# Kernel optimization log

Measured on AMD Instinct MI355X. Metric: run time of the kernel, lower is better.

Reference implementation:

```python
import jax, jax.numpy as jnp
import numpy as np

DEPTH, HEADS, DIM, MLP = 4, 8, 256, 1024
EPS = 1e-5


def setup_inputs() -> dict:
    key = jax.random.key(0)
    ks = jax.random.split(key, 12)
    s = 0.02
    return {
        "x": jax.random.normal(ks[0], (4, 2048, DIM), dtype=jnp.float32),
        "ln1_g": jnp.ones((DEPTH, DIM), jnp.float32),
        "ln1_b": jnp.zeros((DEPTH, DIM), jnp.float32),
        "w_qkv": jax.random.normal(ks[1], (DEPTH, DIM, 3 * DIM), jnp.float32) * s,
        "w_out": jax.random.normal(ks[2], (DEPTH, DIM, DIM), jnp.float32) * s,
        "b_out": jnp.zeros((DEPTH, DIM), jnp.float32),
        "ln2_g": jnp.ones((DEPTH, DIM), jnp.float32),
        "ln2_b": jnp.zeros((DEPTH, DIM), jnp.float32),
        "w1": jax.random.normal(ks[3], (DEPTH, DIM, MLP), jnp.float32) * s,
        "b1": jnp.zeros((DEPTH, MLP), jnp.float32),
        "w2": jax.random.normal(ks[4], (DEPTH, MLP, DIM), jnp.float32) * s,
        "b2": jnp.zeros((DEPTH, DIM), jnp.float32),
    }


def _layernorm(x, g, b):
    m = jnp.mean(x, axis=-1, keepdims=True)
    v = jnp.mean(jnp.square(x - m), axis=-1, keepdims=True)
    return (x - m) * jax.lax.rsqrt(v + EPS) * g + b


def _attention(x, w_qkv, w_out, b_out):
    b, n, d = x.shape
    h = HEADS
    scale = d ** (-0.5)  # NOTE: module scales by dim**-0.5, not head_dim**-0.5
    qkv = x @ w_qkv  # [b, n, 3*d]
    qkv = qkv.reshape(b, n, 3, h, d // h)
    q, k, v = jnp.moveaxis(qkv, 2, 0)  # each [b, n, h, hd]
    q = jnp.swapaxes(q, 1, 2)  # [b, h, n, hd]
    k = jnp.swapaxes(k, 1, 2)
    v = jnp.swapaxes(v, 1, 2)
    dots = jnp.einsum('bhid,bhjd->bhij', q, k) * scale
    attn = jax.nn.softmax(dots, axis=-1)
    out = jnp.einsum('bhij,bhjd->bhid', attn, v)
    out = jnp.swapaxes(out, 1, 2).reshape(b, n, d)
    return out @ w_out + b_out


def _ffn(x, w1, b1, w2, b2):
    return jax.nn.gelu(x @ w1 + b1, approximate=False) @ w2 + b2


def reference(x, ln1_g, ln1_b, w_qkv, w_out, b_out, ln2_g, ln2_b, w1, b1, w2, b2):
    for i in range(DEPTH):
        x = x + _attention(_layernorm(x, ln1_g[i], ln1_b[i]), w_qkv[i], w_out[i], b_out[i])
        x = x + _ffn(_layernorm(x, ln2_g[i], ln2_b[i]), w1[i], b1[i], w2[i], b2[i])
    return x
```

## Files before the change

### kernel.cpp

```cpp
#include <hip/hip_runtime.h>
#include <hip/hip_bf16.h>

#define DEPTH  4
#define NH     8
#define DMODEL 256
#define HD     32
#define MLPD   1024
#define SEQ    2048
#define BATCH  4
#define NTOK   (BATCH*SEQ)

typedef __attribute__((ext_vector_type(8))) short s8v;
typedef __attribute__((ext_vector_type(4))) short s4v;
typedef __attribute__((ext_vector_type(4))) float f4v;
typedef __attribute__((ext_vector_type(16))) float f16v;

#if __has_builtin(__builtin_amdgcn_exp2f)
#define EXP2(x) __builtin_amdgcn_exp2f(x)
#else
#define EXP2(x) exp2f(x)
#endif

__device__ __forceinline__ short f2bf(float f) {
    union { float f; unsigned u; } v; v.f = f;
    unsigned r = v.u + 0x7fffu + ((v.u >> 16) & 1u);
    return (short)(r >> 16);
}

__device__ __forceinline__ f4v mfma16(s8v a, s8v b, f4v c) {
    return __builtin_amdgcn_mfma_f32_16x16x32_bf16(a, b, c, 0, 0, 0);
}
__device__ __forceinline__ f16v mfma32(s8v a, s8v b, f16v c) {
    return __builtin_amdgcn_mfma_f32_32x32x16_bf16(a, b, c, 0, 0, 0);
}

__device__ __forceinline__ void glds16(const short* g, short* l) {
    __builtin_amdgcn_global_load_lds(
        (const __attribute__((address_space(1))) void*)g,
        (__attribute__((address_space(3))) void*)l, 16, 0, 0);
}

#define WAITBAR(NLIT)                                                       \
    do {                                                                    \
        __builtin_amdgcn_sched_barrier(0);                                  \
        asm volatile("s_waitcnt vmcnt(" NLIT ")" ::: "memory");             \
        __builtin_amdgcn_s_barrier();                                       \
        __builtin_amdgcn_sched_barrier(0);                                  \
    } while (0)

__global__ void transpose_cvt(const float* __restrict__ src, short* __restrict__ dst,
                              int K, int N) {
    __shared__ float tile[32][33];
    const int l = blockIdx.z;
    src += (size_t)l * K * N;
    dst += (size_t)l * N * K;
    const int n0 = blockIdx.x * 32, k0 = blockIdx.y * 32;
    const int tx = threadIdx.x, ty = threadIdx.y;
    #pragma unroll
    for (int i = 0; i < 32; i += 8)
        tile[ty + i][tx] = src[(size_t)(k0 + ty + i) * N + n0 + tx];
    __syncthreads();
    #pragma unroll
    for (int i = 0; i < 32; i += 8)
        dst[(size_t)(n0 + ty + i) * K + k0 + tx] = f2bf(tile[tx][ty + i]);
}

__global__ void ln_kernel(const float* __restrict__ x, const float* __restrict__ g,
                          const float* __restrict__ b, short* __restrict__ out) {
    const int row  = blockIdx.x * 4 + (threadIdx.x >> 6);
    const int lane = threadIdx.x & 63;
    const float4 v = *(const float4*)(x + (size_t)row * DMODEL + lane * 4);
    float s = v.x + v.y + v.z + v.w;
    #pragma unroll
    for (int m = 32; m; m >>= 1) s += __shfl_xor(s, m);
    const float mean = s * (1.0f / DMODEL);
    const float dx = v.x - mean, dy = v.y - mean, dz = v.z - mean, dw = v.w - mean;
    float q = dx*dx + dy*dy + dz*dz + dw*dw;
    #pragma unroll
    for (int m = 32; m; m >>= 1) q += __shfl_xor(q, m);
    const float rstd = rsqrtf(q * (1.0f / DMODEL) + 1e-5f);
    const float4 gg = *(const float4*)(g + lane * 4);
    const float4 bb = *(const float4*)(b + lane * 4);
    s4v o;
    o.x = f2bf(dx * rstd * gg.x + bb.x);
    o.y = f2bf(dy * rstd * gg.y + bb.y);
    o.z = f2bf(dz * rstd * gg.z + bb.z);
    o.w = f2bf(dw * rstd * gg.w + bb.w);
    *(s4v*)(out + (size_t)row * DMODEL + lane * 4) = o;
}

#define EPI_QKV  0
#define EPI_RES  1
#define EPI_GELU 2

template<int EPI>
__device__ __forceinline__ void gemm_epilogue(
        f4v acc[2][2], int trow0, int col0, int N, int g, int c,
        const float* __restrict__ bias, float* __restrict__ resio,
        short* __restrict__ outb,
        short* __restrict__ qb, short* __restrict__ kb, short* __restrict__ vtb) {
    if (EPI == EPI_QKV) {
        #pragma unroll
        for (int mf = 0; mf < 2; mf++) {
            const int tokb = trow0 + mf * 16 + g * 4;
            const int b = tokb >> 11, n = tokb & 2047;
            #pragma unroll
            for (int nf = 0; nf < 2; nf++) {
                const int colg = col0 + nf * 16 + c;
                const int part = colg >> 8, pc = colg & 255;
                const int h = pc >> 5, d = pc & 31;
                const size_t bh = (size_t)(b * NH + h);
                if (part == 2) {
                    s4v pv;
                    #pragma unroll
                    for (int r = 0; r < 4; r++) pv[r] = f2bf(acc[mf][nf][r]);
                    *(s4v*)(vtb + (bh * 32 + d) * SEQ + n) = pv;
                } else {
                    const float sc = (part == 0) ? 0.090168440f : 1.0f;
                    short* dst = (part == 0 ? qb : kb) + ((bh << 11) + n) * 32 + d;
                    #pragma unroll
                    for (int r = 0; r < 4; r++) dst[(size_t)r * 32] = f2bf(acc[mf][nf][r] * sc);
                }
            }
        }
    } else if (EPI == EPI_RES) {
        #pragma unroll
        for (int mf = 0; mf < 2; mf++)
            #pragma unroll
            for (int nf = 0; nf < 2; nf++) {
                const int colg = col0 + nf * 16 + c;
                const float bv = bias[colg];
                #pragma unroll
                for (int r = 0; r < 4; r++) {
                    const int row = trow0 + mf * 16 + g * 4 + r;
                    const size_t idx = (size_t)row * N + colg;
                    resio[idx] = resio[idx] + bv + acc[mf][nf][r];
                }
            }
    } else {
        #pragma unroll
        for (int mf = 0; mf < 2; mf++)
            #pragma unroll
            for (int nf = 0; nf < 2; nf++) {
                const int colg = col0 + nf * 16 + c;
                const float bv = bias[colg];
                #pragma unroll
                for (int r = 0; r < 4; r++) {
                    const int row = trow0 + mf * 16 + g * 4 + r;
                    const float v = acc[mf][nf][r] + bv;
                    const float ge = 0.5f * v * (1.0f + erff(v * 0.70710678118f));
                    outb[(size_t)row * N + colg] = f2bf(ge);
                }
            }
    }
}

template<int EPI>
__global__ __launch_bounds__(256) void gemm_p256(
        const short* __restrict__ A, const short* __restrict__ Bt,
        const int N, const int nbx,
        const float* __restrict__ bias,
        float* __restrict__ resio,
        short* __restrict__ outb,
        short* __restrict__ qb, short* __restrict__ kb, short* __restrict__ vtb) {
    __shared__ short ldsA[3][64 * 64];
    __shared__ short ldsB[3][64 * 64];
    const int nblk = gridDim.x;
    const int bid  = blockIdx.x;
    const int swz  = (bid & 7) * (nblk >> 3) + (bid >> 3);
    const int m0 = (swz / nbx) * 64, n0 = (swz % nbx) * 64;
    const int tid  = threadIdx.x;
    const int wave = tid >> 6, lane = tid & 63;
    const int g = lane >> 4, c = lane & 15;
    const int wm = wave >> 1, wn = wave & 1;

#define STAGEP(buf, k0)                                                     \
    do {                                                                    \
        _Pragma("unroll")                                                   \
        for (int i = 0; i < 2; i++) {                                       \
            const int idx = i * 256 + tid;                                  \
            const int row = idx >> 3, c8 = idx & 7;                         \
            const int gcol = (k0) + ((c8 ^ (row & 7)) * 8);                 \
            glds16(A  + (size_t)(m0 + row) * 256 + gcol, &ldsA[buf][idx*8]);\
            glds16(Bt + (size_t)(n0 + row) * 256 + gcol, &ldsB[buf][idx*8]);\
        }                                                                   \
    } while (0)

#define COMPUTE(buf)                                                        \
    do {                                                                    \
        _Pragma("unroll")                                                   \
        for (int kk = 0; kk < 2; kk++) {                                    \
            s8v af[2], bfr[2];                                              \
            _Pragma("unroll")                                               \
            for (int mf = 0; mf < 2; mf++)                                  \
                af[mf] = *(const s8v*)(&ldsA[buf][(wm*32+mf*16+c)*64 +      \
                                        (((kk<<2)+g) ^ (c&7)) * 8]);        \
            _Pragma("unroll")                                               \
            for (int nf = 0; nf < 2; nf++)                                  \
                bfr[nf] = *(const s8v*)(&ldsB[buf][(wn*32+nf*16+c)*64 +     \
                                        (((kk<<2)+g) ^ (c&7)) * 8]);        \
            _Pragma("unroll")                                               \
            for (int mf = 0; mf < 2; mf++)                                  \
                _Pragma("unroll")                                           \
                for (int nf = 0; nf < 2; nf++)                              \
                    acc[mf][nf] = mfma16(af[mf], bfr[nf], acc[mf][nf]);     \
        }                                                                   \
    } while (0)

    f4v acc[2][2];
    #pragma unroll
    for (int i = 0; i < 2; i++)
        #pragma unroll
        for (int j = 0; j < 2; j++) acc[i][j] = (f4v){0.f, 0.f, 0.f, 0.f};

    STAGEP(0, 0);
    STAGEP(1, 64);
    WAITBAR("4");
    STAGEP(2, 128);
    COMPUTE(0);
    WAITBAR("4");
    STAGEP(0, 192);
    COMPUTE(1);
    WAITBAR("4");
    COMPUTE(2);
    WAITBAR("0");
    COMPUTE(0);
#undef STAGEP
#undef COMPUTE

    gemm_epilogue<EPI>(acc, m0 + wm * 32, n0 + wn * 32, N, g, c,
                       bias, resio, outb, qb, kb, vtb);
}

template<int KTOT, int EPI>
__global__ __launch_bounds__(256) void gemm_bt2(
        const short* __restrict__ A, const short* __restrict__ Bt,
        const int N, const int nbx,
        const float* __restrict__ bias,
        float* __restrict__ resio,
        short* __restrict__ outb) {
    __shared__ short ldsA[2][64 * 64];
    __shared__ short ldsB[2][64 * 64];
    const int nblk = gridDim.x;
    const int bid  = blockIdx.x;
    const int swz  = (bid & 7) * (nblk >> 3) + (bid >> 3);
    const int m0 = (swz / nbx) * 64, n0 = (swz % nbx) * 64;
    const int tid  = threadIdx.x;
    const int wave = tid >> 6, lane = tid & 63;
    const int g = lane >> 4, c = lane & 15;
    const int wm = wave >> 1, wn = wave & 1;
    const int srow = tid >> 3;
    const int sc8  = (tid & 7) ^ (srow & 7);

    f4v acc[2][2];
    #pragma unroll
    for (int i = 0; i < 2; i++)
        #pragma unroll
        for (int j = 0; j < 2; j++) acc[i][j] = (f4v){0.f, 0.f, 0.f, 0.f};

#define STAGE2(buf, k0)                                                     \
    do {                                                                    \
        glds16(A  + (size_t)(m0 + srow) * KTOT + (k0) + sc8 * 8,            \
               &ldsA[buf][tid * 8]);                                        \
        glds16(A  + (size_t)(m0 + 32 + srow) * KTOT + (k0) + sc8 * 8,       \
               &ldsA[buf][2048 + tid * 8]);                                 \
        glds16(Bt + (size_t)(n0 + srow) * KTOT + (k0) + sc8 * 8,            \
               &ldsB[buf][tid * 8]);                                        \
        glds16(Bt + (size_t)(n0 + 32 + srow) * KTOT + (k0) + sc8 * 8,       \
               &ldsB[buf][2048 + tid * 8]);                                 \
    } while (0)

    STAGE2(0, 0);
    __syncthreads();
    int cur = 0;
    for (int k0 = 0; k0 < KTOT; k0 += 64) {
        if (k0 + 64 < KTOT) STAGE2(cur ^ 1, k0 + 64);
        #pragma unroll
        for (int kk = 0; kk < 2; kk++) {
            s8v af[2], bfr[2];
            #pragma unroll
            for (int mf = 0; mf < 2; mf++)
                af[mf] = *(const s8v*)(&ldsA[cur][(wm*32+mf*16+c)*64 +
                                        (((kk<<2)+g) ^ (c&7)) * 8]);
            #pragma unroll
            for (int nf = 0; nf < 2; nf++)
                bfr[nf] = *(const s8v*)(&ldsB[cur][(wn*32+nf*16+c)*64 +
                                        (((kk<<2)+g) ^ (c&7)) * 8]);
            #pragma unroll
            for (int mf = 0; mf < 2; mf++)
                #pragma unroll
                for (int nf = 0; nf < 2; nf++)
                    acc[mf][nf] = mfma16(af[mf], bfr[nf], acc[mf][nf]);
        }
        __syncthreads();
        cur ^= 1;
    }
#undef STAGE2

    gemm_epilogue<EPI>(acc, m0 + wm * 32, n0 + wn * 32, N, g, c,
                       bias, resio, outb, nullptr, nullptr, nullptr);
}

__global__ __launch_bounds__(256) void attn_kernel(
        const short* __restrict__ qb, const short* __restrict__ kb,
        const short* __restrict__ vtb, short* __restrict__ out) {
    __shared__ short ldsK[3][2048];
    __shared__ short ldsV[3][2048];
    const int bh = blockIdx.y;
    const int tid = threadIdx.x;
    const int wave = tid >> 6, lane = tid & 63;
    const int ql = lane & 31;
    const int h2 = lane >> 5;
    const int q0 = blockIdx.x * 128 + wave * 32;
    const short* Q  = qb  + (size_t)bh * SEQ * HD;
    const short* Kp = kb  + (size_t)bh * SEQ * HD;
    const short* Vt = vtb + (size_t)bh * HD * SEQ;

    const s8v qf1 = *(const s8v*)(Q + (size_t)(q0 + ql) * HD + 8 * h2);
    const s8v qf2 = *(const s8v*)(Q + (size_t)(q0 + ql) * HD + 16 + 8 * h2);
    const s8v ones = (s8v){0x3F80,0x3F80,0x3F80,0x3F80,0x3F80,0x3F80,0x3F80,0x3F80};

    const f16v zero = {};
    f16v o   = zero;
    f16v lsv = zero;

    const short* gK = Kp + (size_t)(tid & 63) * HD + (tid >> 6) * 8;
    const short* gV = Vt + (size_t)(tid & 31) * SEQ + (tid >> 5) * 8;

#define ASTAGE(buf, kt)                                                     \
    do {                                                                    \
        glds16(gK + (size_t)(kt) * HD, &ldsK[buf][tid * 8]);                \
        glds16(gV + (kt),              &ldsV[buf][tid * 8]);                \
    } while (0)

#define ACOMPUTE(buf)                                                       \
    do {                                                                    \
        _Pragma("unroll")                                                   \
        for (int kk = 0; kk < 2; kk++) {                                    \
            const s8v ka1 = *(const s8v*)(&ldsK[buf][(kk*32 + ql + 64*h2) * 8]);        \
            const s8v ka2 = *(const s8v*)(&ldsK[buf][(kk*32 + ql + 128 + 64*h2) * 8]);  \
            f16v s = mfma32(ka1, qf1, zero);                                \
            s = mfma32(ka2, qf2, s);                                        \
            float p[16];                                                    \
            _Pragma("unroll")                                               \
            for (int r = 0; r < 16; r++) p[r] = EXP2(s[r]);                 \
            int w[8];                                                       \
            _Pragma("unroll")                                               \
            for (int i = 0; i < 8; i++) {                                   \
                union { __hip_bfloat162 h; int i32; } u;                    \
                u.h = __float22bfloat162_rn(float2{p[2*i], p[2*i+1]});      \
                w[i] = u.i32;                                               \
            }                                                               \
            asm("v_permlane32_swap_b32 %0, %1" : "+v"(w[0]), "+v"(w[2]));   \
            asm("v_permlane32_swap_b32 %0, %1" : "+v"(w[1]), "+v"(w[3]));   \
            asm("v_permlane32_swap_b32 %0, %1" : "+v"(w[4]), "+v"(w[6]));   \
            asm("v_permlane32_swap_b32 %0, %1" : "+v"(w[5]), "+v"(w[7]));   \
            union { int i[4]; s8v v; } B1, B2;                              \
            B1.i[0]=w[0]; B1.i[1]=w[1]; B1.i[2]=w[2]; B1.i[3]=w[3];         \
            B2.i[0]=w[4]; B2.i[1]=w[5]; B2.i[2]=w[6]; B2.i[3]=w[7];         \
            lsv = mfma32(ones, B1.v, lsv);                                  \
            lsv = mfma32(ones, B2.v, lsv);                                  \
            const s8v va1 = *(const s8v*)(&ldsV[buf][(ql + 128*kk + 32*h2) * 8]);       \
            const s8v va2 = *(const s8v*)(&ldsV[buf][(ql + 128*kk + 64 + 32*h2) * 8]);  \
            o = mfma32(va1, B1.v, o);                                       \
            o = mfma32(va2, B2.v, o);                                       \
        }                                                                   \
    } while (0)

    int b0 = 0, b1 = 1, b2 = 2;
    ASTAGE(0, 0);
    ASTAGE(1, 64);
    WAITBAR("2");
    for (int t = 0; t < 32; ++t) {
        if (t + 2 < 32) ASTAGE(b2, (t + 2) * 64);
        ACOMPUTE(b0);
        if (t + 2 < 32)      WAITBAR("2");
        else if (t == 30)    WAITBAR("0");
        const int tmp = b0; b0 = b1; b1 = b2; b2 = tmp;
    }
#undef ASTAGE
#undef ACOMPUTE

    const int b = bh >> 3, hh = bh & 7;
    const float inv = 1.0f / lsv[0];
    const size_t rowoff = (size_t)(b * SEQ + q0 + ql) * DMODEL + hh * HD;
    #pragma unroll
    for (int rr = 0; rr < 4; rr++) {
        union { __hip_bfloat162 h2v[2]; s4v v; } uo;
        uo.h2v[0] = __float22bfloat162_rn(float2{o[4*rr]   * inv, o[4*rr+1] * inv});
        uo.h2v[1] = __float22bfloat162_rn(float2{o[4*rr+2] * inv, o[4*rr+3] * inv});
        *(s4v*)(out + rowoff + 8 * rr + 4 * h2) = uo.v;
    }
}

extern "C" void kernel_launch(void* const* d_in, const int* in_sizes, int n_in,
                              void* d_out, int out_size, void* d_ws, size_t ws_size,
                              hipStream_t stream) {
    const float* w_qkv = (const float*)d_in[3];
    const float* w_out = (const float*)d_in[4];
    const float* b_out = (const float*)d_in[5];
    const float* w1    = (const float*)d_in[8];
    const float* b1    = (const float*)d_in[9];
    const float* w2    = (const float*)d_in[10];
    const float* b2    = (const float*)d_in[11];
    const float* ln1_g = (const float*)d_in[1];
    const float* ln1_b = (const float*)d_in[2];
    const float* ln2_g = (const float*)d_in[6];
    const float* ln2_b = (const float*)d_in[7];
    float* xout = (float*)d_out;

    short* ws    = (short*)d_ws;
    short* xn    = ws;
    short* qb    = xn    + (size_t)NTOK * DMODEL;
    short* kb    = qb    + (size_t)BATCH * NH * SEQ * HD;
    short* vtb   = kb    + (size_t)BATCH * NH * SEQ * HD;
    short* ao    = vtb   + (size_t)BATCH * NH * SEQ * HD;
    short* mid   = ao    + (size_t)NTOK * DMODEL;
    short* wqkvT = mid   + (size_t)NTOK * MLPD;
    short* woutT = wqkvT + (size_t)DEPTH * 3 * DMODEL * DMODEL;
    short* w1T   = woutT + (size_t)DEPTH * DMODEL * DMODEL;
    short* w2T   = w1T   + (size_t)DEPTH * MLPD * DMODEL;

    hipMemcpyAsync(d_out, d_in[0], (size_t)NTOK * DMODEL * sizeof(float),
                   hipMemcpyDeviceToDevice, stream);

    transpose_cvt<<<dim3(3*DMODEL/32, DMODEL/32, DEPTH), dim3(32, 8), 0, stream>>>(
        w_qkv, wqkvT, DMODEL, 3*DMODEL);
    transpose_cvt<<<dim3(DMODEL/32, DMODEL/32, DEPTH), dim3(32, 8), 0, stream>>>(
        w_out, woutT, DMODEL, DMODEL);
    transpose_cvt<<<dim3(MLPD/32, DMODEL/32, DEPTH), dim3(32, 8), 0, stream>>>(
        w1, w1T, DMODEL, MLPD);
    transpose_cvt<<<dim3(DMODEL/32, MLPD/32, DEPTH), dim3(32, 8), 0, stream>>>(
        w2, w2T, MLPD, DMODEL);

    for (int l = 0; l < DEPTH; l++) {
        ln_kernel<<<NTOK/4, 256, 0, stream>>>(xout, ln1_g + l*DMODEL, ln1_b + l*DMODEL, xn);
        gemm_p256<EPI_QKV><<<1536, 256, 0, stream>>>(
            xn, wqkvT + (size_t)l * 3 * DMODEL * DMODEL,
            3*DMODEL, 12, nullptr, nullptr, nullptr, qb, kb, vtb);
        attn_kernel<<<dim3(SEQ/128, BATCH*NH), 256, 0, stream>>>(qb, kb, vtb, ao);
        gemm_p256<EPI_RES><<<512, 256, 0, stream>>>(
            ao, woutT + (size_t)l * DMODEL * DMODEL,
            DMODEL, 4, b_out + l*DMODEL, xout, nullptr, nullptr, nullptr, nullptr);
        ln_kernel<<<NTOK/4, 256, 0, stream>>>(xout, ln2_g + l*DMODEL, ln2_b + l*DMODEL, xn);
        gemm_p256<EPI_GELU><<<2048, 256, 0, stream>>>(
            xn, w1T + (size_t)l * MLPD * DMODEL,
            MLPD, 16, b1 + l*MLPD, nullptr, mid, nullptr, nullptr, nullptr);
        gemm_bt2<1024, EPI_RES><<<512, 256, 0, stream>>>(
            mid, w2T + (size_t)l * DMODEL * MLPD,
            DMODEL, 4, b2 + l*DMODEL, xout, nullptr);
    }
}
```

Measured before the change: 425.5 us.

## Restructure attention kernel into 2-wave blocks with double-buffered 128-key stages

Attention blocks shrink from 4 waves/128 queries to 2 waves/64 queries, doubling the grid. The K/V pipeline changes from a triple buffer of 64-key tiles to a double buffer of 128-key tiles (two sub-tiles per stage), with a full wait each iteration. Compute sections are wrapped in s_setprio to favor MFMA issue. This aims to raise occupancy and cut per-tile barrier overhead, but each block now reuses staged K/V across only two waves and the loop waits for all loads each step.

After: 445.5 us. 1.05x slower.

```diff
diff --git a/kernel.cpp b/kernel.cpp
--- a/kernel.cpp
+++ b/kernel.cpp
@@ -301,17 +301,17 @@
                        bias, resio, outb, nullptr, nullptr, nullptr);
 }
 
-__global__ __launch_bounds__(256) void attn_kernel(
+__global__ __launch_bounds__(128) void attn_kernel(
         const short* __restrict__ qb, const short* __restrict__ kb,
         const short* __restrict__ vtb, short* __restrict__ out) {
-    __shared__ short ldsK[3][2048];
-    __shared__ short ldsV[3][2048];
+    __shared__ short ldsK[2][512 * 8];
+    __shared__ short ldsV[2][512 * 8];
     const int bh = blockIdx.y;
     const int tid = threadIdx.x;
     const int wave = tid >> 6, lane = tid & 63;
     const int ql = lane & 31;
     const int h2 = lane >> 5;
-    const int q0 = blockIdx.x * 128 + wave * 32;
+    const int q0 = blockIdx.x * 64 + wave * 32;
     const short* Q  = qb  + (size_t)bh * SEQ * HD;
     const short* Kp = kb  + (size_t)bh * SEQ * HD;
     const short* Vt = vtb + (size_t)bh * HD * SEQ;
@@ -324,21 +324,27 @@
     f16v o   = zero;
     f16v lsv = zero;
 
-    const short* gK = Kp + (size_t)(tid & 63) * HD + (tid >> 6) * 8;
-    const short* gV = Vt + (size_t)(tid & 31) * SEQ + (tid >> 5) * 8;
-
 #define ASTAGE(buf, kt)                                                     \
     do {                                                                    \
-        glds16(gK + (size_t)(kt) * HD, &ldsK[buf][tid * 8]);                \
-        glds16(gV + (kt),              &ldsV[buf][tid * 8]);                \
-    } while (0)
-
-#define ACOMPUTE(buf)                                                       \
+        _Pragma("unroll")                                                   \
+        for (int j = 0; j < 4; j++) {                                       \
+            const int s2 = tid + 128 * j;                                   \
+            const int ti = s2 >> 8, s = s2 & 255;                           \
+            glds16(Kp + (size_t)((kt) + ti * 64 + (s & 63)) * HD            \
+                       + ((s >> 6) & 3) * 8,                                \
+                   &ldsK[buf][s2 * 8]);                                     \
+            glds16(Vt + (size_t)(s & 31) * SEQ + ((s >> 5) & 7) * 8         \
+                       + (kt) + ti * 64,                                    \
+                   &ldsV[buf][s2 * 8]);                                     \
+        }                                                                   \
+    } while (0)
+
+#define ATILE(buf, ti)                                                      \
     do {                                                                    \
         _Pragma("unroll")                                                   \
         for (int kk = 0; kk < 2; kk++) {                                    \
-            const s8v ka1 = *(const s8v*)(&ldsK[buf][(kk*32 + ql + 64*h2) * 8]);        \
-            const s8v ka2 = *(const s8v*)(&ldsK[buf][(kk*32 + ql + 128 + 64*h2) * 8]);  \
+            const s8v ka1 = *(const s8v*)(&ldsK[buf][((ti)*256 + kk*32 + ql + 64*h2) * 8]);        \
+            const s8v ka2 = *(const s8v*)(&ldsK[buf][((ti)*256 + kk*32 + ql + 128 + 64*h2) * 8]);  \
             f16v s = mfma32(ka1, qf1, zero);                                \
             s = mfma32(ka2, qf2, s);                                        \
             float p[16];                                                    \
@@ -360,26 +366,27 @@
             B2.i[0]=w[4]; B2.i[1]=w[5]; B2.i[2]=w[6]; B2.i[3]=w[7];         \
             lsv = mfma32(ones, B1.v, lsv);                                  \
             lsv = mfma32(ones, B2.v, lsv);                                  \
-            const s8v va1 = *(const s8v*)(&ldsV[buf][(ql + 128*kk + 32*h2) * 8]);       \
-            const s8v va2 = *(const s8v*)(&ldsV[buf][(ql + 128*kk + 64 + 32*h2) * 8]);  \
+            const s8v va1 = *(const s8v*)(&ldsV[buf][((ti)*256 + ql + 128*kk + 32*h2) * 8]);       \
+            const s8v va2 = *(const s8v*)(&ldsV[buf][((ti)*256 + ql + 128*kk + 64 + 32*h2) * 8]);  \
             o = mfma32(va1, B1.v, o);                                       \
             o = mfma32(va2, B2.v, o);                                       \
         }                                                                   \
     } while (0)
 
-    int b0 = 0, b1 = 1, b2 = 2;
     ASTAGE(0, 0);
-    ASTAGE(1, 64);
-    WAITBAR("2");
-    for (int t = 0; t < 32; ++t) {
-        if (t + 2 < 32) ASTAGE(b2, (t + 2) * 64);
-        ACOMPUTE(b0);
-        if (t + 2 < 32)      WAITBAR("2");
-        else if (t == 30)    WAITBAR("0");
-        const int tmp = b0; b0 = b1; b1 = b2; b2 = tmp;
+    WAITBAR("0");
+    int cur = 0;
+    for (int p = 0; p < 16; ++p) {
+        if (p < 15) ASTAGE(cur ^ 1, (p + 1) * 128);
+        __builtin_amdgcn_s_setprio(1);
+        ATILE(cur, 0);
+        ATILE(cur, 1);
+        __builtin_amdgcn_s_setprio(0);
+        if (p < 15) WAITBAR("0");
+        cur ^= 1;
     }
 #undef ASTAGE
-#undef ACOMPUTE
+#undef ATILE
 
     const int b = bh >> 3, hh = bh & 7;
     const float inv = 1.0f / lsv[0];
@@ -438,7 +445,7 @@
         gemm_p256<EPI_QKV><<<1536, 256, 0, stream>>>(
             xn, wqkvT + (size_t)l * 3 * DMODEL * DMODEL,
             3*DMODEL, 12, nullptr, nullptr, nullptr, qb, kb, vtb);
-        attn_kernel<<<dim3(SEQ/128, BATCH*NH), 256, 0, stream>>>(qb, kb, vtb, ao);
+        attn_kernel<<<dim3(SEQ/64, BATCH*NH), 128, 0, stream>>>(qb, kb, vtb, ao);
         gemm_p256<EPI_RES><<<512, 256, 0, stream>>>(
             ao, woutT + (size_t)l * DMODEL * DMODEL,
             DMODEL, 4, b_out + l*DMODEL, xout, nullptr, nullptr, nullptr, nullptr);
```

## Replace pipelined 64x64 GEMMs with single-buffered larger-tile unified GEMM template

Applied to the files above, without the earlier changes.

Replaces the triple-buffered and double-buffered 64x64 GEMM kernels with one templated kernel that uses 128x128 or 128x64 tiles and a single LDS buffer, with a barrier before and after each K step. The larger tiles give each block more MFMA work per staged byte and launch fewer blocks, aiming to raise data reuse. In exchange, the overlap between global-to-LDS loads and compute is lost. The grids also shrink to 256-512 blocks, which may underfill the GPU's CUs.

Measured after the change: 442.5 us. 1.04x slower.

```diff
diff --git a/kernel.cpp b/kernel.cpp
--- a/kernel.cpp
+++ b/kernel.cpp
@@ -93,19 +93,78 @@
 #define EPI_RES  1
 #define EPI_GELU 2
 
-template<int EPI>
-__device__ __forceinline__ void gemm_epilogue(
-        f4v acc[2][2], int trow0, int col0, int N, int g, int c,
-        const float* __restrict__ bias, float* __restrict__ resio,
+template<int BM, int BN, int KTOT, int EPI>
+__global__ __launch_bounds__(256) void gemm_s(
+        const short* __restrict__ A, const short* __restrict__ Bt,
+        const int N, const int nbx,
+        const float* __restrict__ bias,
+        float* __restrict__ resio,
         short* __restrict__ outb,
         short* __restrict__ qb, short* __restrict__ kb, short* __restrict__ vtb) {
+    constexpr int FM = BM / 32, FN = BN / 32;
+    __shared__ short ldsA[BM * 64];
+    __shared__ short ldsB[BN * 64];
+    const int nblk = gridDim.x;
+    const int bid  = blockIdx.x;
+    const int swz  = (bid & 7) * (nblk >> 3) + (bid >> 3);
+    const int m0 = (swz / nbx) * BM, n0 = (swz % nbx) * BN;
+    const int tid  = threadIdx.x;
+    const int wave = tid >> 6, lane = tid & 63;
+    const int g = lane >> 4, c = lane & 15;
+    const int wm = wave >> 1, wn = wave & 1;
+
+    f4v acc[FM][FN];
+    #pragma unroll
+    for (int i = 0; i < FM; i++)
+        #pragma unroll
+        for (int j = 0; j < FN; j++) acc[i][j] = (f4v){0.f, 0.f, 0.f, 0.f};
+
+    for (int k0 = 0; k0 < KTOT; k0 += 64) {
+        #pragma unroll
+        for (int i = 0; i < BM / 32; i++) {
+            const int idx = i * 256 + tid;
+            const int row = idx >> 3, c8 = idx & 7;
+            glds16(A + (size_t)(m0 + row) * KTOT + k0 + ((c8 ^ (row & 7)) * 8),
+                   &ldsA[idx * 8]);
+        }
+        #pragma unroll
+        for (int i = 0; i < BN / 32; i++) {
+            const int idx = i * 256 + tid;
+            const int row = idx >> 3, c8 = idx & 7;
+            glds16(Bt + (size_t)(n0 + row) * KTOT + k0 + ((c8 ^ (row & 7)) * 8),
+                   &ldsB[idx * 8]);
+        }
+        __syncthreads();
+        #pragma unroll
+        for (int kk = 0; kk < 2; kk++) {
+            s8v af[FM], bfr[FN];
+            #pragma unroll
+            for (int mf = 0; mf < FM; mf++)
+                af[mf] = *(const s8v*)(&ldsA[(wm * (BM/2) + mf * 16 + c) * 64 +
+                                             (((kk << 2) + g) ^ (c & 7)) * 8]);
+            #pragma unroll
+            for (int nf = 0; nf < FN; nf++)
+                bfr[nf] = *(const s8v*)(&ldsB[(wn * (BN/2) + nf * 16 + c) * 64 +
+                                              (((kk << 2) + g) ^ (c & 7)) * 8]);
+            #pragma unroll
+            for (int mf = 0; mf < FM; mf++)
+                #pragma unroll
+                for (int nf = 0; nf < FN; nf++)
+                    acc[mf][nf] = mfma16(af[mf], bfr[nf], acc[mf][nf]);
+        }
+        __syncthreads();
+    }
+
+    const int trow0 = m0 + wm * (BM/2);
+    const int col0  = n0 + wn * (BN/2);
+
     if (EPI == EPI_QKV) {
         #pragma unroll
-        for (int mf = 0; mf < 2; mf++) {
+        for (int mf = 0; mf < FM; mf++) {
             const int tokb = trow0 + mf * 16 + g * 4;
             const int b = tokb >> 11, n = tokb & 2047;
             #pragma unroll
-            for (int nf = 0; nf < 2; nf++) {
+            for (int nf = 0; nf < FN; nf++) {
                 const int colg = col0 + nf * 16 + c;
                 const int part = colg >> 8, pc = colg & 255;
                 const int h = pc >> 5, d = pc & 31;
@@ -125,9 +184,9 @@
         }
     } else if (EPI == EPI_RES) {
         #pragma unroll
-        for (int mf = 0; mf < 2; mf++)
-            #pragma unroll
-            for (int nf = 0; nf < 2; nf++) {
+        for (int mf = 0; mf < FM; mf++)
+            #pragma unroll
+            for (int nf = 0; nf < FN; nf++) {
                 const int colg = col0 + nf * 16 + c;
                 const float bv = bias[colg];
                 #pragma unroll
@@ -139,9 +198,9 @@
             }
     } else {
         #pragma unroll
-        for (int mf = 0; mf < 2; mf++)
-            #pragma unroll
-            for (int nf = 0; nf < 2; nf++) {
+        for (int mf = 0; mf < FM; mf++)
+            #pragma unroll
+            for (int nf = 0; nf < FN; nf++) {
                 const int colg = col0 + nf * 16 + c;
                 const float bv = bias[colg];
                 #pragma unroll
@@ -153,152 +212,6 @@
                 }
             }
     }
-}
-
-template<int EPI>
-__global__ __launch_bounds__(256) void gemm_p256(
-        const short* __restrict__ A, const short* __restrict__ Bt,
-        const int N, const int nbx,
-        const float* __restrict__ bias,
-        float* __restrict__ resio,
-        short* __restrict__ outb,
-        short* __restrict__ qb, short* __restrict__ kb, short* __restrict__ vtb) {
-    __shared__ short ldsA[3][64 * 64];
-    __shared__ short ldsB[3][64 * 64];
-    const int nblk = gridDim.x;
-    const int bid  = blockIdx.x;
-    const int swz  = (bid & 7) * (nblk >> 3) + (bid >> 3);
-    const int m0 = (swz / nbx) * 64, n0 = (swz % nbx) * 64;
-    const int tid  = threadIdx.x;
-    const int wave = tid >> 6, lane = tid & 63;
-    const int g = lane >> 4, c = lane & 15;
-    const int wm = wave >> 1, wn = wave & 1;
-
-#define STAGEP(buf, k0)                                                     \
-    do {                                                                    \
-        _Pragma("unroll")                                                   \
-        for (int i = 0; i < 2; i++) {                                       \
-            const int idx = i * 256 + tid;                                  \
-            const int row = idx >> 3, c8 = idx & 7;                         \
-            const int gcol = (k0) + ((c8 ^ (row & 7)) * 8);                 \
-            glds16(A  + (size_t)(m0 + row) * 256 + gcol, &ldsA[buf][idx*8]);\
-            glds16(Bt + (size_t)(n0 + row) * 256 + gcol, &ldsB[buf][idx*8]);\
-        }                                                                   \
-    } while (0)
-
-#define COMPUTE(buf)                                                        \
-    do {                                                                    \
-        _Pragma("unroll")                                                   \
-        for (int kk = 0; kk < 2; kk++) {                                    \
-            s8v af[2], bfr[2];                                              \
-            _Pragma("unroll")                                               \
-            for (int mf = 0; mf < 2; mf++)                                  \
-                af[mf] = *(const s8v*)(&ldsA[buf][(wm*32+mf*16+c)*64 +      \
-                                        (((kk<<2)+g) ^ (c&7)) * 8]);        \
-            _Pragma("unroll")                                               \
-            for (int nf = 0; nf < 2; nf++)                                  \
-                bfr[nf] = *(const s8v*)(&ldsB[buf][(wn*32+nf*16+c)*64 +     \
-                                        (((kk<<2)+g) ^ (c&7)) * 8]);        \
-            _Pragma("unroll")                                               \
-            for (int mf = 0; mf < 2; mf++)                                  \
-                _Pragma("unroll")                                           \
-                for (int nf = 0; nf < 2; nf++)                              \
-                    acc[mf][nf] = mfma16(af[mf], bfr[nf], acc[mf][nf]);     \
-        }                                                                   \
-    } while (0)
-
-    f4v acc[2][2];
-    #pragma unroll
-    for (int i = 0; i < 2; i++)
-        #pragma unroll
-        for (int j = 0; j < 2; j++) acc[i][j] = (f4v){0.f, 0.f, 0.f, 0.f};
-
-    STAGEP(0, 0);
-    STAGEP(1, 64);
-    WAITBAR("4");
-    STAGEP(2, 128);
-    COMPUTE(0);
-    WAITBAR("4");
-    STAGEP(0, 192);
-    COMPUTE(1);
-    WAITBAR("4");
-    COMPUTE(2);
-    WAITBAR("0");
-    COMPUTE(0);
-#undef STAGEP
-#undef COMPUTE
-
-    gemm_epilogue<EPI>(acc, m0 + wm * 32, n0 + wn * 32, N, g, c,
-                       bias, resio, outb, qb, kb, vtb);
-}
-
-template<int KTOT, int EPI>
-__global__ __launch_bounds__(256) void gemm_bt2(
-        const short* __restrict__ A, const short* __restrict__ Bt,
-        const int N, const int nbx,
-        const float* __restrict__ bias,
-        float* __restrict__ resio,
-        short* __restrict__ outb) {
-    __shared__ short ldsA[2][64 * 64];
-    __shared__ short ldsB[2][64 * 64];
-    const int nblk = gridDim.x;
-    const int bid  = blockIdx.x;
-    const int swz  = (bid & 7) * (nblk >> 3) + (bid >> 3);
-    const int m0 = (swz / nbx) * 64, n0 = (swz % nbx) * 64;
-    const int tid  = threadIdx.x;
-    const int wave = tid >> 6, lane = tid & 63;
-    const int g = lane >> 4, c = lane & 15;
-    const int wm = wave >> 1, wn = wave & 1;
-    const int srow = tid >> 3;
-    const int sc8  = (tid & 7) ^ (srow & 7);
-
-    f4v acc[2][2];
-    #pragma unroll
-    for (int i = 0; i < 2; i++)
-        #pragma unroll
-        for (int j = 0; j < 2; j++) acc[i][j] = (f4v){0.f, 0.f, 0.f, 0.f};
-
-#define STAGE2(buf, k0)                                                     \
-    do {                                                                    \
-        glds16(A  + (size_t)(m0 + srow) * KTOT + (k0) + sc8 * 8,            \
-               &ldsA[buf][tid * 8]);                                        \
-        glds16(A  + (size_t)(m0 + 32 + srow) * KTOT + (k0) + sc8 * 8,       \
-               &ldsA[buf][2048 + tid * 8]);                                 \
-        glds16(Bt + (size_t)(n0 + srow) * KTOT + (k0) + sc8 * 8,            \
-               &ldsB[buf][tid * 8]);                                        \
-        glds16(Bt + (size_t)(n0 + 32 + srow) * KTOT + (k0) + sc8 * 8,       \
-               &ldsB[buf][2048 + tid * 8]);                                 \
-    } while (0)
-
-    STAGE2(0, 0);
-    __syncthreads();
-    int cur = 0;
-    for (int k0 = 0; k0 < KTOT; k0 += 64) {
-        if (k0 + 64 < KTOT) STAGE2(cur ^ 1, k0 + 64);
-        #pragma unroll
-        for (int kk = 0; kk < 2; kk++) {
-            s8v af[2], bfr[2];
-            #pragma unroll
-            for (int mf = 0; mf < 2; mf++)
-                af[mf] = *(const s8v*)(&ldsA[cur][(wm*32+mf*16+c)*64 +
-                                        (((kk<<2)+g) ^ (c&7)) * 8]);
-            #pragma unroll
-            for (int nf = 0; nf < 2; nf++)
-                bfr[nf] = *(const s8v*)(&ldsB[cur][(wn*32+nf*16+c)*64 +
-                                        (((kk<<2)+g) ^ (c&7)) * 8]);
-            #pragma unroll
-            for (int mf = 0; mf < 2; mf++)
-                #pragma unroll
-                for (int nf = 0; nf < 2; nf++)
-                    acc[mf][nf] = mfma16(af[mf], bfr[nf], acc[mf][nf]);
-        }
-        __syncthreads();
-        cur ^= 1;
-    }
-#undef STAGE2
-
-    gemm_epilogue<EPI>(acc, m0 + wm * 32, n0 + wn * 32, N, g, c,
-                       bias, resio, outb, nullptr, nullptr, nullptr);
 }
 
 __global__ __launch_bounds__(256) void attn_kernel(
@@ -435,19 +348,19 @@
 
     for (int l = 0; l < DEPTH; l++) {
         ln_kernel<<<NTOK/4, 256, 0, stream>>>(xout, ln1_g + l*DMODEL, ln1_b + l*DMODEL, xn);
-        gemm_p256<EPI_QKV><<<1536, 256, 0, stream>>>(
+        gemm_s<128,128,256,EPI_QKV><<<384, 256, 0, stream>>>(
             xn, wqkvT + (size_t)l * 3 * DMODEL * DMODEL,
-            3*DMODEL, 12, nullptr, nullptr, nullptr, qb, kb, vtb);
+            3*DMODEL, 6, nullptr, nullptr, nullptr, qb, kb, vtb);
         attn_kernel<<<dim3(SEQ/128, BATCH*NH), 256, 0, stream>>>(qb, kb, vtb, ao);
-        gemm_p256<EPI_RES><<<512, 256, 0, stream>>>(
+        gemm_s<128,64,256,EPI_RES><<<256, 256, 0, stream>>>(
             ao, woutT + (size_t)l * DMODEL * DMODEL,
             DMODEL, 4, b_out + l*DMODEL, xout, nullptr, nullptr, nullptr, nullptr);
         ln_kernel<<<NTOK/4, 256, 0, stream>>>(xout, ln2_g + l*DMODEL, ln2_b + l*DMODEL, xn);
-        gemm_p256<EPI_GELU><<<2048, 256, 0, stream>>>(
+        gemm_s<128,128,256,EPI_GELU><<<512, 256, 0, stream>>>(
             xn, w1T + (size_t)l * MLPD * DMODEL,
-            MLPD, 16, b1 + l*MLPD, nullptr, mid, nullptr, nullptr, nullptr);
-        gemm_bt2<1024, EPI_RES><<<512, 256, 0, stream>>>(
+            MLPD, 8, b1 + l*MLPD, nullptr, mid, nullptr, nullptr, nullptr);
+        gemm_s<128,64,1024,EPI_RES><<<256, 256, 0, stream>>>(
             mid, w2T + (size_t)l * DMODEL * MLPD,
-            DMODEL, 4, b2 + l*DMODEL, xout, nullptr);
-    }
-}
+            DMODEL, 4, b2 + l*DMODEL, xout, nullptr, nullptr, nullptr, nullptr);
+    }
+}
```
